# Performance work log

Hardware: AMD Instinct MI355X
Metric: run time of the kernel (lower is better)

The kernel has to match this reference:

```python
import jax, jax.numpy as jnp
import numpy as np

EPS_BN = 1e-5  # torch BatchNorm1d default eps


def setup_inputs() -> dict:
    key = jax.random.key(0)
    k1, k2, k3 = jax.random.split(key, 3)
    B, C, L = 512, 8, 16384
    attn_maps = jax.random.normal(k1, (B, C, L), dtype=jnp.float32)
    target_matrix = jax.random.uniform(k2, (B, C, C), dtype=jnp.float32)
    conv_bias = jnp.ones((C,), dtype=jnp.float32) * 0.5  # nn.Parameter(torch.ones(8)/2)
    w_fc = jax.random.normal(k3, (3, 1), dtype=jnp.float32) * 0.1
    b_fc = jnp.zeros((3,), dtype=jnp.float32)
    return {"attn_maps": attn_maps, "target_matrix": target_matrix,
            "conv_bias": conv_bias, "w_fc": w_fc, "b_fc": b_fc}


def reference(attn_maps, target_matrix, conv_bias, w_fc, b_fc):
    B, C, L = attn_maps.shape  # C == 8 (fixed by the grouped 1x1 conv)
    # (attn - mean of per-row means) * 100; rows are uniform length so this is the global mean
    x = (attn_maps - jnp.mean(attn_maps)) * 100.0
    # grouped conv1d, kernel 1, weight == 5: per-channel affine, then sigmoid / 5
    bin_maps = jax.nn.sigmoid(5.0 * x + conv_bias[None, :, None]) / 5.0  # (B, C, L)
    b5 = bin_maps * 5.0
    # vectorized triangular IoU: intersection / union over the length dim
    inter = jnp.einsum('bil,bjl->bij', b5, b5)                     # (B, C, C)
    union = L - jnp.einsum('bil,bjl->bij', 1.0 - b5, 1.0 - b5)      # (B, C, C)
    tril = jnp.tril(jnp.ones((C, C), dtype=bool))
    sim = jnp.where(tril, inter / union, 0.0)
    # rep_type 'abs': sum of |sim - 100*target| over the lower triangle (incl. diag)
    tm = target_matrix * 100.0
    st = jnp.sum(jnp.where(tril, jnp.abs(sim - tm), 0.0), axis=(1, 2))  # (B,)
    # BatchNorm1d(1, affine=False) in training mode: normalize over the batch
    mu = jnp.mean(st)
    var = jnp.var(st)  # biased variance, as torch BN uses for normalization
    st_n = (st - mu) * jax.lax.rsqrt(var + EPS_BN)                  # (B,)
    # final linear 1 -> 3 (original Linear(128,3) is shape-inconsistent; see notes)
    out = st_n[:, None] @ w_fc.T + b_fc                              # (B, 3)
    return out
```

## Files before the change

### kernel.cpp

```cpp
#include <hip/hip_runtime.h>
#include <math.h>

typedef float f32x4 __attribute__((ext_vector_type(4)));
typedef _Float16 f16x2 __attribute__((ext_vector_type(2)));

#define B_DIM 512
#define C_DIM 8
#define L_DIM 16384
#define NELEM (B_DIM * C_DIM * L_DIM)
#define LOG2E 1.4426950408889634f
#define KA (-500.0f * LOG2E)

#if __has_builtin(__builtin_amdgcn_exp2f)
#define EXP2F __builtin_amdgcn_exp2f
#else
#define EXP2F exp2f
#endif

#if __has_builtin(__builtin_amdgcn_fdot2)
#define HAVE_FDOT2 1
#else
#define HAVE_FDOT2 0
#endif

#define H_NODE 0.25
#define F_P 1.2840254166877414f
#define F_M 0.7788007830714049f

#define TRI(i, j) ((i) * ((i) + 1) / 2 + (j))

#define WS_GRAM_OFF 8192

typedef const __attribute__((address_space(1))) unsigned int gu32_t;
typedef __attribute__((address_space(3))) unsigned int lu32_t;
__device__ __forceinline__ void gload_lds16(const void* g, void* l) {
  __builtin_amdgcn_global_load_lds((gu32_t*)g, (lu32_t*)l, 16, 0, 0);
}

__global__ __launch_bounds__(256) void k_main(const f32x4* __restrict__ in4,
                                              const float* __restrict__ bias,
                                              float* __restrict__ asum,
                                              float* __restrict__ gram_t) {
  const int tid = threadIdx.x;
  const int lane = tid & 63, wv = tid >> 6;
  const int nodesel = tid >> 7;
  const int pt = tid & 127;
  const int b = blockIdx.x;

  __shared__ char smem[49152];

  const float Fn = nodesel ? F_M : F_P;
  float kc[C_DIM];
#pragma unroll
  for (int c = 0; c < C_DIM; ++c) kc[c] = bias[c] * (-LOG2E);

  float acc[44];
#pragma unroll
  for (int k = 0; k < 44; ++k) acc[k] = 0.f;
  float asacc = 0.f;

#if HAVE_FDOT2
  const f16x2 ONE2 = {(_Float16)1.f, (_Float16)1.f};
#endif

  const size_t gbase = (size_t)b * (C_DIM * 4096);

  auto stage = [&](int it, int d) {
#pragma unroll
    for (int k = 0; k < 4; ++k) {
      const int c = 2 * k + (tid >> 7);
      const f32x4* g = in4 + gbase + (size_t)c * 4096 + it * 128 + pt;
      char* l = smem + d * 16384 + k * 4096 + wv * 1024;
      gload_lds16((const void*)g, (void*)l);
    }
  };

  auto compute = [&](const f32x4* v) {
#pragma unroll
    for (int p = 0; p < 2; ++p) {
      float sx[C_DIM], sy[C_DIM];
#if HAVE_FDOT2
      f16x2 s2[C_DIM];
#endif
#pragma unroll
      for (int c = 0; c < C_DIM; ++c) {
        const float ax = p ? v[c].z : v[c].x;
        const float ay = p ? v[c].w : v[c].y;
        if (nodesel == 0) asacc += ax + ay;
        const float Ex = EXP2F(fmaf(KA, ax, kc[c]));
        const float Ey = EXP2F(fmaf(KA, ay, kc[c]));
        sx[c] = __builtin_amdgcn_rcpf(fmaf(Ex, Fn, 1.f));
        sy[c] = __builtin_amdgcn_rcpf(fmaf(Ey, Fn, 1.f));
#if HAVE_FDOT2
        s2[c] = __builtin_bit_cast(f16x2, __builtin_amdgcn_cvt_pkrtz(sx[c], sy[c]));
        acc[c] = __builtin_amdgcn_fdot2(s2[c], ONE2, acc[c], false);
#else
        acc[c] += sx[c] + sy[c];
#endif
      }
#pragma unroll
      for (int i = 0; i < C_DIM; ++i)
#pragma unroll
        for (int j = 0; j <= i; ++j) {
#if HAVE_FDOT2
          acc[8 + TRI(i, j)] =
              __builtin_amdgcn_fdot2(s2[i], s2[j], acc[8 + TRI(i, j)], false);
#else
          acc[8 + TRI(i, j)] =
              fmaf(sx[i], sx[j], fmaf(sy[i], sy[j], acc[8 + TRI(i, j)]));
#endif
        }
    }
  };

  auto consume = [&](int d) {
    const char* lb = smem + d * 16384;
    f32x4 v[C_DIM];
#pragma unroll
    for (int c = 0; c < C_DIM; ++c)
      v[c] = *(const f32x4*)(lb + (c >> 1) * 4096 + (c & 1) * 2048 + pt * 16);
    compute(v);
  };

  stage(0, 0);
  stage(1, 1);
  stage(2, 2);

#pragma unroll 1
  for (int it = 0; it < 30; ++it) {
    const int d = it % 3;
    asm volatile("s_waitcnt vmcnt(8)" ::: "memory");
    __builtin_amdgcn_s_barrier();
    consume(d);
    __builtin_amdgcn_s_barrier();
    if (it < 29) stage(it + 3, d);
  }
  asm volatile("s_waitcnt vmcnt(4)" ::: "memory");
  __builtin_amdgcn_s_barrier();
  consume(0);
  __builtin_amdgcn_s_barrier();
  asm volatile("s_waitcnt vmcnt(0)" ::: "memory");
  __builtin_amdgcn_s_barrier();
  consume(1);

  __shared__ float lgr[4][44];
  __shared__ float las[2];
#pragma unroll
  for (int k = 0; k < 44; ++k) {
    float x = acc[k];
#pragma unroll
    for (int off = 32; off; off >>= 1) x += __shfl_xor(x, off, 64);
    if (lane == 0) lgr[wv][k] = x;
  }
  if (nodesel == 0) {
    float x = asacc;
#pragma unroll
    for (int off = 32; off; off >>= 1) x += __shfl_xor(x, off, 64);
    if (lane == 0) las[wv] = x;
  }
  __syncthreads();
  if (tid < 88) {
    const int n = tid / 44, k = tid - n * 44;
    gram_t[(size_t)(n * 44 + k) * 512 + b] = lgr[2 * n][k] + lgr[2 * n + 1][k];
  }
  if (tid == 96) asum[b] = las[0] + las[1];
}

__global__ __launch_bounds__(512) void k_final(const float* __restrict__ asum,
                                               const float* __restrict__ gram_t,
                                               const float* __restrict__ target,
                                               const float* __restrict__ w_fc,
                                               const float* __restrict__ b_fc,
                                               float* __restrict__ out) {
  const int t = threadIdx.x;
  __shared__ double red[512];

  red[t] = (double)asum[t];
  __syncthreads();
  for (int off = 256; off; off >>= 1) {
    if (t < off) red[t] += red[t + off];
    __syncthreads();
  }
  const double th = 500.0 * (red[0] / (double)NELEM);
  __syncthreads();

  const double w0 = (th + H_NODE) / (2.0 * H_NODE);
  const double w1 = (H_NODE - th) / (2.0 * H_NODE);

  const float* g = gram_t + t;
  double S[8], T[36];
#pragma unroll
  for (int i = 0; i < 8; ++i)
    S[i] = w0 * (double)g[(0 + i) * 512] + w1 * (double)g[(44 + i) * 512];
#pragma unroll
  for (int k = 0; k < 36; ++k)
    T[k] = w0 * (double)g[(8 + k) * 512] + w1 * (double)g[(52 + k) * 512];

  double st = 0.0;
#pragma unroll
  for (int i = 0; i < 8; ++i)
#pragma unroll
    for (int j = 0; j <= i; ++j) {
      double inter = T[TRI(i, j)];
      double uni = (S[i] + S[j]) - inter;
      double sim = inter / uni;
      double tm = 100.0 * (double)target[t * 64 + i * 8 + j];
      st += fabs(sim - tm);
    }

  red[t] = st;
  __syncthreads();
  for (int off = 256; off; off >>= 1) {
    if (t < off) red[t] += red[t + off];
    __syncthreads();
  }
  const double mean = red[0] * (1.0 / 512.0);
  __syncthreads();
  const double dd = st - mean;
  red[t] = dd * dd;
  __syncthreads();
  for (int off = 256; off; off >>= 1) {
    if (t < off) red[t] += red[t + off];
    __syncthreads();
  }
  const double var = red[0] * (1.0 / 512.0);
  const float stn = (float)((st - mean) / sqrt(var + 1e-5));
#pragma unroll
  for (int k = 0; k < 3; ++k)
    out[t * 3 + k] = fmaf(stn, w_fc[k], b_fc[k]);
}

extern "C" void kernel_launch(void* const* d_in, const int* in_sizes, int n_in,
                              void* d_out, int out_size, void* d_ws, size_t ws_size,
                              hipStream_t stream) {
  const float* attn   = (const float*)d_in[0];
  const float* target = (const float*)d_in[1];
  const float* bias   = (const float*)d_in[2];
  const float* w_fc   = (const float*)d_in[3];
  const float* b_fc   = (const float*)d_in[4];
  float* out = (float*)d_out;
  float* ws  = (float*)d_ws;

  float* asum   = ws;
  float* gram_t = ws + WS_GRAM_OFF;

  k_main<<<B_DIM, 256, 0, stream>>>((const f32x4*)attn, bias, asum, gram_t);
  k_final<<<1, 512, 0, stream>>>(asum, gram_t, target, w_fc, b_fc, out);
}
```

Measured before the change: 81.39 us.

## Restructure LDS staging into double-buffered larger tiles with per-wave channel loads

Replaces the triple-buffered 16KB-stage pipeline with a double-buffered 32KB-tile pipeline. Each wave loads two whole channels per tile, 16 loads in flight per thread, and each tile is consumed in two sub-steps. This cuts the number of barrier pairs per block in half and makes each wave's global reads contiguous per channel. The cost is more LDS per block (64KB), which may lower occupancy, and the prefetch depth drops to one tile ahead.

```diff
diff --git a/kernel.cpp b/kernel.cpp
--- a/kernel.cpp
+++ b/kernel.cpp
@@ -30,6 +30,11 @@
 #define TRI(i, j) ((i) * ((i) + 1) / 2 + (j))
 
 #define WS_GRAM_OFF 8192
+
+#define NT 16
+#define T4 256
+#define CH4 4096
+#define TILE_B 32768
 
 typedef const __attribute__((address_space(1))) unsigned int gu32_t;
 typedef __attribute__((address_space(3))) unsigned int lu32_t;
@@ -47,7 +52,7 @@
   const int pt = tid & 127;
   const int b = blockIdx.x;
 
-  __shared__ char smem[49152];
+  __shared__ char smem[2 * TILE_B];
 
   const float Fn = nodesel ? F_M : F_P;
   float kc[C_DIM];
@@ -63,15 +68,18 @@
   const f16x2 ONE2 = {(_Float16)1.f, (_Float16)1.f};
 #endif
 
-  const size_t gbase = (size_t)b * (C_DIM * 4096);
-
-  auto stage = [&](int it, int d) {
-#pragma unroll
-    for (int k = 0; k < 4; ++k) {
-      const int c = 2 * k + (tid >> 7);
-      const f32x4* g = in4 + gbase + (size_t)c * 4096 + it * 128 + pt;
-      char* l = smem + d * 16384 + k * 4096 + wv * 1024;
-      gload_lds16((const void*)g, (void*)l);
+  const size_t gbase = (size_t)b * (C_DIM * CH4);
+
+  auto stage = [&](int t, int d) {
+#pragma unroll
+    for (int ci = 0; ci < 2; ++ci) {
+      const int c = 2 * wv + ci;
+#pragma unroll
+      for (int q = 0; q < 4; ++q) {
+        const f32x4* g = in4 + gbase + (size_t)c * CH4 + t * T4 + q * 64 + lane;
+        char* l = smem + d * TILE_B + c * 4096 + q * 1024;
+        gload_lds16((const void*)g, (void*)l);
+      }
     }
   };
 
@@ -114,34 +122,35 @@
   };
 
   auto consume = [&](int d) {
-    const char* lb = smem + d * 16384;
-    f32x4 v[C_DIM];
-#pragma unroll
-    for (int c = 0; c < C_DIM; ++c)
-      v[c] = *(const f32x4*)(lb + (c >> 1) * 4096 + (c & 1) * 2048 + pt * 16);
-    compute(v);
+    const char* lb = smem + d * TILE_B;
+#pragma unroll
+    for (int sub = 0; sub < 2; ++sub) {
+      f32x4 v[C_DIM];
+#pragma unroll
+      for (int c = 0; c < C_DIM; ++c)
+        v[c] = *(const f32x4*)(lb + c * 4096 + (sub * 128 + pt) * 16);
+      compute(v);
+    }
   };
 
   stage(0, 0);
   stage(1, 1);
-  stage(2, 2);
 
 #pragma unroll 1
-  for (int it = 0; it < 30; ++it) {
-    const int d = it % 3;
-    asm volatile("s_waitcnt vmcnt(8)" ::: "memory");
+  for (int t = 0; t < NT; ++t) {
+    const int d = t & 1;
+    if (t + 2 < NT) {
+      asm volatile("s_waitcnt vmcnt(8)" ::: "memory");
+    } else if (t + 1 < NT) {
+      asm volatile("s_waitcnt vmcnt(8)" ::: "memory");
+    } else {
+      asm volatile("s_waitcnt vmcnt(0)" ::: "memory");
+    }
     __builtin_amdgcn_s_barrier();
     consume(d);
     __builtin_amdgcn_s_barrier();
-    if (it < 29) stage(it + 3, d);
-  }
-  asm volatile("s_waitcnt vmcnt(4)" ::: "memory");
-  __builtin_amdgcn_s_barrier();
-  consume(0);
-  __builtin_amdgcn_s_barrier();
-  asm volatile("s_waitcnt vmcnt(0)" ::: "memory");
-  __builtin_amdgcn_s_barrier();
-  consume(1);
+    if (t + 2 < NT) stage(t + 2, d);
+  }
 
   __shared__ float lgr[4][44];
   __shared__ float las[2];
```

Result: no change. 82.42 us (+1.3%).
